# Performance work log

Hardware: AMD Instinct MI355X
Metric: run time of the kernel (lower is better)

The kernel has to match this reference:

```python
import jax, jax.numpy as jnp
import numpy as np

B, F, D, H = 2048, 32, 64, 64

def setup_inputs() -> dict:
    key = jax.random.key(0)
    k1, k2, k3 = jax.random.split(key, 3)
    x = jax.random.normal(k1, (B, F, D), dtype=jnp.float32)
    W1 = jax.random.normal(k2, (D, H), dtype=jnp.float32) * 0.01
    b1 = jnp.zeros((H,), dtype=jnp.float32)
    Ws = jax.random.normal(k3, (H, 1), dtype=jnp.float32) * 0.01
    bs = jnp.zeros((1,), dtype=jnp.float32)
    return {"x": x, "W1": W1, "b1": b1, "Ws": Ws, "bs": bs}

def reference(x, W1, b1, Ws, bs):
    # pairwise field interactions: cross[b, p, d] = x[b, i_p, d] * x[b, j_p, d]
    f = x.shape[1]
    ii, jj = np.triu_indices(f, k=1)  # P = f*(f-1)/2 pairs
    cross = x[:, ii, :] * x[:, jj, :]            # [B, P, D]
    # small MLP (DNN with one hidden layer, relu, dropout disabled in eval)
    h = jax.nn.relu(jnp.einsum('bpd,dh->bph', cross, W1) + b1)  # [B, P, H]
    # attention score per pair, softmax over pairs
    scores = (jnp.einsum('bph,ho->bpo', h, Ws) + bs).squeeze(-1)  # [B, P]
    attn = jax.nn.softmax(scores, axis=-1)                        # [B, P]
    pool = jnp.sum(cross * attn[:, :, None], axis=1)              # [B, D]
    afm = jnp.sum(pool, axis=1, keepdims=True)                    # [B, 1]
    return afm
```

## Files before the change

### kernel.cpp

```cpp
#include <hip/hip_runtime.h>


#define F 32
#define D 64
#define H 64
#define P 496
#define NT 4
#define MT 32
#define RB 72

typedef __attribute__((ext_vector_type(8))) _Float16 f16x8;
typedef __attribute__((ext_vector_type(2))) _Float16 f16x2;
typedef __attribute__((ext_vector_type(4))) float f32x4;

__global__ __launch_bounds__(256, 4) void afm_kernel(
    const float* __restrict__ x, const float* __restrict__ W1,
    const float* __restrict__ b1, const float* __restrict__ Ws,
    const float* __restrict__ bs, float* __restrict__ out)
{
    __shared__ _Float16 xs[F * RB];
    __shared__ int   pairtab[512];
    __shared__ float scores[512];
    __shared__ float svals[512];
    __shared__ float redmax[4], rednum[4], redden[4];

    const int tid  = threadIdx.x;
    const int b    = blockIdx.x;
    const int lane = tid & 63;
    const int wid  = tid >> 6;
    const int l15  = lane & 15;
    const int quad = lane >> 4;

    const float4* xb4 = (const float4*)(x + (size_t)b * (F * D));
    for (int v = tid; v < (F * D) / 4; v += 256) {
        float4 w = xb4[v];
        int row = v >> 4, col = (v & 15) * 4;
        f16x2 lo = { (_Float16)w.x, (_Float16)w.y };
        f16x2 hi = { (_Float16)w.z, (_Float16)w.w };
        *(f16x2*)&xs[row * RB + col]     = lo;
        *(f16x2*)&xs[row * RB + col + 2] = hi;
    }
    for (int p = tid; p < 512; p += 256) {
        int i, j;
        if (p < P) {
            i = (int)((63.0f - __builtin_sqrtf((float)(3969 - 8 * p))) * 0.5f);
            if (i * (63 - i) / 2 > p) --i;
            if ((i + 1) * (62 - i) / 2 <= p) ++i;
            j = i + 1 + (p - i * (63 - i) / 2);
        } else { i = 0; j = 0; }
        pairtab[p] = (i * RB * 2) << 16 | (j * RB * 2);
    }
    const float bsv = bs[0];

    f16x8 wfrag[NT][2];
    #pragma unroll
    for (int nt = 0; nt < NT; ++nt)
        #pragma unroll
        for (int ks = 0; ks < 2; ++ks)
            #pragma unroll
            for (int j8 = 0; j8 < 8; ++j8) {
                int k = quad * 8 + j8 + ks * 32;
                wfrag[nt][ks][j8] = (_Float16)W1[k * H + nt * 16 + l15];
            }
    const _Float16 onev = (l15 == 0) ? (_Float16)1.0f : (_Float16)0.0f;
    const f16x8 onesf = {onev, onev, onev, onev, onev, onev, onev, onev};

    float breg[16], wreg[16];
    #pragma unroll
    for (int nt = 0; nt < NT; ++nt)
        #pragma unroll
        for (int reg = 0; reg < 4; ++reg) {
            int n = nt * 16 + quad * 4 + reg;
            breg[nt * 4 + reg] = b1[n];
            wreg[nt * 4 + reg] = Ws[n];
        }
    __syncthreads();

    const char* xsb = (const char*)xs;
    const int qb = quad << 4;

    for (int t = wid; t < MT; t += 4) {
        const int p0 = t * 16;
        const int pk = pairtab[p0 + l15];
        const int io = ((unsigned)pk) >> 16;
        const int jo = pk & 0xFFFF;

        f16x8 xi0 = *(const f16x8*)(xsb + io + qb);
        f16x8 xj0 = *(const f16x8*)(xsb + jo + qb);
        f16x8 xi1 = *(const f16x8*)(xsb + io + 64 + qb);
        f16x8 xj1 = *(const f16x8*)(xsb + jo + 64 + qb);

        f16x8 A0 = xi0 * xj0;
        f16x8 A1 = xi1 * xj1;

        f32x4 acc[NT];
        #pragma unroll
        for (int nt = 0; nt < NT; ++nt) { f32x4 z = {0.f,0.f,0.f,0.f}; acc[nt] = z; }
        f32x4 accs = {0.f, 0.f, 0.f, 0.f};

        #pragma unroll
        for (int nt = 0; nt < NT; ++nt)
            acc[nt] = __builtin_amdgcn_mfma_f32_16x16x32_f16(wfrag[nt][0], A0, acc[nt], 0, 0, 0);
        accs = __builtin_amdgcn_mfma_f32_16x16x32_f16(onesf, A0, accs, 0, 0, 0);
        #pragma unroll
        for (int nt = 0; nt < NT; ++nt)
            acc[nt] = __builtin_amdgcn_mfma_f32_16x16x32_f16(wfrag[nt][1], A1, acc[nt], 0, 0, 0);
        accs = __builtin_amdgcn_mfma_f32_16x16x32_f16(onesf, A1, accs, 0, 0, 0);

        float s = 0.f;
        #pragma unroll
        for (int nt = 0; nt < NT; ++nt)
            #pragma unroll
            for (int reg = 0; reg < 4; ++reg) {
                float v = acc[nt][reg] + breg[nt * 4 + reg];
                v = v > 0.f ? v : 0.f;
                s = fmaf(v, wreg[nt * 4 + reg], s);
            }
        s += __shfl_xor(s, 16, 64);
        s += __shfl_xor(s, 32, 64);
        if (quad == 0) {
            scores[p0 + l15] = s + bsv;
            svals[p0 + l15]  = accs[0];
        }
    }
    __syncthreads();

    float m = -1e30f;
    for (int p = tid; p < P; p += 256) m = fmaxf(m, scores[p]);
    #pragma unroll
    for (int off = 32; off >= 1; off >>= 1) m = fmaxf(m, __shfl_xor(m, off, 64));
    if (lane == 0) redmax[wid] = m;
    __syncthreads();
    m = fmaxf(fmaxf(redmax[0], redmax[1]), fmaxf(redmax[2], redmax[3]));

    float num = 0.f, den = 0.f;
    for (int p = tid; p < P; p += 256) {
        float e = __expf(scores[p] - m);
        num += e * svals[p];
        den += e;
    }
    #pragma unroll
    for (int off = 32; off >= 1; off >>= 1) {
        num += __shfl_xor(num, off, 64);
        den += __shfl_xor(den, off, 64);
    }
    if (lane == 0) { rednum[wid] = num; redden[wid] = den; }
    __syncthreads();
    if (tid == 0) {
        float nn = rednum[0] + rednum[1] + rednum[2] + rednum[3];
        float dd = redden[0] + redden[1] + redden[2] + redden[3];
        out[b] = nn / dd;
    }
}

extern "C" void kernel_launch(void* const* d_in, const int* in_sizes, int n_in,
                              void* d_out, int out_size, void* d_ws, size_t ws_size,
                              hipStream_t stream) {
    const float* x  = (const float*)d_in[0];
    const float* W1 = (const float*)d_in[1];
    const float* b1 = (const float*)d_in[2];
    const float* Ws = (const float*)d_in[3];
    const float* bs = (const float*)d_in[4];
    float* out = (float*)d_out;
    const int B = in_sizes[0] / (F * D);
    afm_kernel<<<B, 256, 0, stream>>>(x, W1, b1, Ws, bs, out);
}
```

Baseline: 83.91 us.

## Restructure pair loop over row-i tiles and drop max-subtracted softmax

Replaces the shared-memory staging of x and the pair table with direct global loads into registers. Each wave iterates over row i and builds 16-column j tiles of products, masking out pairs with j <= i. The separate max pass of the softmax is removed, so exp is applied to raw scores and num/den are accumulated in registers without score buffers or most barriers. This cuts LDS traffic and synchronisation but computes some masked pairs that are thrown away, and drops overflow protection in the exponent, relying on scores staying small.

```diff
diff --git a/kernel.cpp b/kernel.cpp
--- a/kernel.cpp
+++ b/kernel.cpp
@@ -4,25 +4,16 @@
 #define F 32
 #define D 64
 #define H 64
-#define P 496
-#define NT 4
-#define MT 32
-#define RB 72
 
 typedef __attribute__((ext_vector_type(8))) _Float16 f16x8;
-typedef __attribute__((ext_vector_type(2))) _Float16 f16x2;
 typedef __attribute__((ext_vector_type(4))) float f32x4;
 
-__global__ __launch_bounds__(256, 4) void afm_kernel(
+__global__ __launch_bounds__(256, 3) void afm_kernel(
     const float* __restrict__ x, const float* __restrict__ W1,
     const float* __restrict__ b1, const float* __restrict__ Ws,
     const float* __restrict__ bs, float* __restrict__ out)
 {
-    __shared__ _Float16 xs[F * RB];
-    __shared__ int   pairtab[512];
-    __shared__ float scores[512];
-    __shared__ float svals[512];
-    __shared__ float redmax[4], rednum[4], redden[4];
+    __shared__ float rednum[4], redden[4];
 
     const int tid  = threadIdx.x;
     const int b    = blockIdx.x;
@@ -31,116 +22,104 @@
     const int l15  = lane & 15;
     const int quad = lane >> 4;
 
-    const float4* xb4 = (const float4*)(x + (size_t)b * (F * D));
-    for (int v = tid; v < (F * D) / 4; v += 256) {
-        float4 w = xb4[v];
-        int row = v >> 4, col = (v & 15) * 4;
-        f16x2 lo = { (_Float16)w.x, (_Float16)w.y };
-        f16x2 hi = { (_Float16)w.z, (_Float16)w.w };
-        *(f16x2*)&xs[row * RB + col]     = lo;
-        *(f16x2*)&xs[row * RB + col + 2] = hi;
-    }
-    for (int p = tid; p < 512; p += 256) {
-        int i, j;
-        if (p < P) {
-            i = (int)((63.0f - __builtin_sqrtf((float)(3969 - 8 * p))) * 0.5f);
-            if (i * (63 - i) / 2 > p) --i;
-            if ((i + 1) * (62 - i) / 2 <= p) ++i;
-            j = i + 1 + (p - i * (63 - i) / 2);
-        } else { i = 0; j = 0; }
-        pairtab[p] = (i * RB * 2) << 16 | (j * RB * 2);
-    }
-    const float bsv = bs[0];
-
-    f16x8 wfrag[NT][2];
+    f16x8 wfrag[4][2];
     #pragma unroll
-    for (int nt = 0; nt < NT; ++nt)
+    for (int nt = 0; nt < 4; ++nt)
         #pragma unroll
         for (int ks = 0; ks < 2; ++ks)
             #pragma unroll
-            for (int j8 = 0; j8 < 8; ++j8) {
-                int k = quad * 8 + j8 + ks * 32;
-                wfrag[nt][ks][j8] = (_Float16)W1[k * H + nt * 16 + l15];
-            }
+            for (int j8 = 0; j8 < 8; ++j8)
+                wfrag[nt][ks][j8] =
+                    (_Float16)W1[(quad * 8 + j8 + 32 * ks) * H + nt * 16 + l15];
+
     const _Float16 onev = (l15 == 0) ? (_Float16)1.0f : (_Float16)0.0f;
     const f16x8 onesf = {onev, onev, onev, onev, onev, onev, onev, onev};
 
     float breg[16], wreg[16];
     #pragma unroll
-    for (int nt = 0; nt < NT; ++nt)
+    for (int nt = 0; nt < 4; ++nt)
         #pragma unroll
         for (int reg = 0; reg < 4; ++reg) {
             int n = nt * 16 + quad * 4 + reg;
             breg[nt * 4 + reg] = b1[n];
             wreg[nt * 4 + reg] = Ws[n];
         }
-    __syncthreads();
+    const float bsv = bs[0];
 
-    const char* xsb = (const char*)xs;
-    const int qb = quad << 4;
+    const float* xb = x + (size_t)b * (F * D);
+    f16x8 xjf[2][2];
+    #pragma unroll
+    for (int J = 0; J < 2; ++J)
+        #pragma unroll
+        for (int ks = 0; ks < 2; ++ks) {
+            const float* src = xb + (J * 16 + l15) * D + quad * 8 + 32 * ks;
+            float4 a = *(const float4*)src;
+            float4 c = *(const float4*)(src + 4);
+            f16x8 v;
+            v[0] = (_Float16)a.x; v[1] = (_Float16)a.y;
+            v[2] = (_Float16)a.z; v[3] = (_Float16)a.w;
+            v[4] = (_Float16)c.x; v[5] = (_Float16)c.y;
+            v[6] = (_Float16)c.z; v[7] = (_Float16)c.w;
+            xjf[J][ks] = v;
+        }
 
-    for (int t = wid; t < MT; t += 4) {
-        const int p0 = t * 16;
-        const int pk = pairtab[p0 + l15];
-        const int io = ((unsigned)pk) >> 16;
-        const int jo = pk & 0xFFFF;
+    float num = 0.f, den = 0.f;
 
-        f16x8 xi0 = *(const f16x8*)(xsb + io + qb);
-        f16x8 xj0 = *(const f16x8*)(xsb + jo + qb);
-        f16x8 xi1 = *(const f16x8*)(xsb + io + 64 + qb);
-        f16x8 xj1 = *(const f16x8*)(xsb + jo + 64 + qb);
+    for (int ii = 0; ii < 8; ++ii) {
+        const int i = wid + 4 * ii;
 
-        f16x8 A0 = xi0 * xj0;
-        f16x8 A1 = xi1 * xj1;
+        f16x8 xi16[2];
+        #pragma unroll
+        for (int ks = 0; ks < 2; ++ks) {
+            const float* src = xb + i * D + quad * 8 + 32 * ks;
+            float4 a = *(const float4*)src;
+            float4 c = *(const float4*)(src + 4);
+            f16x8 v;
+            v[0] = (_Float16)a.x; v[1] = (_Float16)a.y;
+            v[2] = (_Float16)a.z; v[3] = (_Float16)a.w;
+            v[4] = (_Float16)c.x; v[5] = (_Float16)c.y;
+            v[6] = (_Float16)c.z; v[7] = (_Float16)c.w;
+            xi16[ks] = v;
+        }
 
-        f32x4 acc[NT];
-        #pragma unroll
-        for (int nt = 0; nt < NT; ++nt) { f32x4 z = {0.f,0.f,0.f,0.f}; acc[nt] = z; }
-        f32x4 accs = {0.f, 0.f, 0.f, 0.f};
+        for (int Jp = (i < 16) ? 0 : 1; Jp < 2; ++Jp) {
+            f32x4 acc[4];
+            #pragma unroll
+            for (int nt = 0; nt < 4; ++nt) { f32x4 z = {0.f,0.f,0.f,0.f}; acc[nt] = z; }
+            f32x4 accs = {0.f, 0.f, 0.f, 0.f};
 
-        #pragma unroll
-        for (int nt = 0; nt < NT; ++nt)
-            acc[nt] = __builtin_amdgcn_mfma_f32_16x16x32_f16(wfrag[nt][0], A0, acc[nt], 0, 0, 0);
-        accs = __builtin_amdgcn_mfma_f32_16x16x32_f16(onesf, A0, accs, 0, 0, 0);
-        #pragma unroll
-        for (int nt = 0; nt < NT; ++nt)
-            acc[nt] = __builtin_amdgcn_mfma_f32_16x16x32_f16(wfrag[nt][1], A1, acc[nt], 0, 0, 0);
-        accs = __builtin_amdgcn_mfma_f32_16x16x32_f16(onesf, A1, accs, 0, 0, 0);
+            #pragma unroll
+            for (int ks = 0; ks < 2; ++ks) {
+                f16x8 B = xjf[Jp][ks] * xi16[ks];
+                #pragma unroll
+                for (int nt = 0; nt < 4; ++nt)
+                    acc[nt] = __builtin_amdgcn_mfma_f32_16x16x32_f16(
+                                  wfrag[nt][ks], B, acc[nt], 0, 0, 0);
+                accs = __builtin_amdgcn_mfma_f32_16x16x32_f16(onesf, B, accs, 0, 0, 0);
+            }
 
-        float s = 0.f;
-        #pragma unroll
-        for (int nt = 0; nt < NT; ++nt)
+            float s = 0.f;
             #pragma unroll
-            for (int reg = 0; reg < 4; ++reg) {
-                float v = acc[nt][reg] + breg[nt * 4 + reg];
-                v = v > 0.f ? v : 0.f;
-                s = fmaf(v, wreg[nt * 4 + reg], s);
-            }
-        s += __shfl_xor(s, 16, 64);
-        s += __shfl_xor(s, 32, 64);
-        if (quad == 0) {
-            scores[p0 + l15] = s + bsv;
-            svals[p0 + l15]  = accs[0];
+            for (int nt = 0; nt < 4; ++nt)
+                #pragma unroll
+                for (int reg = 0; reg < 4; ++reg) {
+                    float v = acc[nt][reg] + breg[nt * 4 + reg];
+                    v = v > 0.f ? v : 0.f;
+                    s = fmaf(v, wreg[nt * 4 + reg], s);
+                }
+            s += __shfl_xor(s, 16, 64);
+            s += __shfl_xor(s, 32, 64);
+
+            float e = __expf(s + bsv);
+            const int j = Jp * 16 + l15;
+            e = (quad == 0 && j > i) ? e : 0.f;
+            num = fmaf(e, accs[0], num);
+            den += e;
         }
     }
-    __syncthreads();
 
-    float m = -1e30f;
-    for (int p = tid; p < P; p += 256) m = fmaxf(m, scores[p]);
     #pragma unroll
-    for (int off = 32; off >= 1; off >>= 1) m = fmaxf(m, __shfl_xor(m, off, 64));
-    if (lane == 0) redmax[wid] = m;
-    __syncthreads();
-    m = fmaxf(fmaxf(redmax[0], redmax[1]), fmaxf(redmax[2], redmax[3]));
-
-    float num = 0.f, den = 0.f;
-    for (int p = tid; p < P; p += 256) {
-        float e = __expf(scores[p] - m);
-        num += e * svals[p];
-        den += e;
-    }
-    #pragma unroll
-    for (int off = 32; off >= 1; off >>= 1) {
+    for (int off = 8; off >= 1; off >>= 1) {
         num += __shfl_xor(num, off, 64);
         den += __shfl_xor(den, off, 64);
     }
```

Measured after the change: 95.05 us. +13.3%, slower.

## Fuse softmax into MFMA loop, stage W1 fragments via LDS, pack bias math

Applied to the files above, without the earlier changes.

Drops the max-subtraction pass and the scores/svals shared arrays. Exp and the numerator/denominator sums are now accumulated directly inside the pair loop, which removes two block barriers and the extra LDS passes. W1 is loaded once with coalesced float4 reads into a fragment-ordered LDS buffer instead of strided scalar global loads per lane. The bias, relu and score step uses packed float2 math. Skipping max subtraction risks overflow in exp if scores grow large; with the small weights in the test inputs the scores stay near zero.

```diff
diff --git a/kernel.cpp b/kernel.cpp
--- a/kernel.cpp
+++ b/kernel.cpp
@@ -5,13 +5,13 @@
 #define D 64
 #define H 64
 #define P 496
-#define NT 4
 #define MT 32
 #define RB 72
 
 typedef __attribute__((ext_vector_type(8))) _Float16 f16x8;
 typedef __attribute__((ext_vector_type(2))) _Float16 f16x2;
 typedef __attribute__((ext_vector_type(4))) float f32x4;
+typedef __attribute__((ext_vector_type(2))) float f32x2;
 
 __global__ __launch_bounds__(256, 4) void afm_kernel(
     const float* __restrict__ x, const float* __restrict__ W1,
@@ -19,10 +19,10 @@
     const float* __restrict__ bs, float* __restrict__ out)
 {
     __shared__ _Float16 xs[F * RB];
-    __shared__ int   pairtab[512];
-    __shared__ float scores[512];
-    __shared__ float svals[512];
-    __shared__ float redmax[4], rednum[4], redden[4];
+    __shared__ _Float16 w1f[4096];
+    __shared__ float2 bw[H];
+    __shared__ int pairtab[512];
+    __shared__ float rednum[4], redden[4];
 
     const int tid  = threadIdx.x;
     const int b    = blockIdx.x;
@@ -40,6 +40,22 @@
         *(f16x2*)&xs[row * RB + col]     = lo;
         *(f16x2*)&xs[row * RB + col + 2] = hi;
     }
+    const float4* w14 = (const float4*)W1;
+    #pragma unroll
+    for (int s = 0; s < 4; ++s) {
+        int v = tid + s * 256;
+        float4 w = w14[v];
+        int k  = v >> 4;
+        int ks = k >> 5, kq = (k >> 3) & 3, j8 = k & 7;
+        int n0 = (v & 15) * 4;
+        float e4[4] = { w.x, w.y, w.z, w.w };
+        #pragma unroll
+        for (int c = 0; c < 4; ++c) {
+            int n = n0 + c, nt = n >> 4, l = n & 15;
+            w1f[(((ks * 4 + nt) * 16 + l) * 4 + kq) * 8 + j8] = (_Float16)e4[c];
+        }
+    }
+    if (tid < H) bw[tid] = make_float2(b1[tid], Ws[tid]);
     for (int p = tid; p < 512; p += 256) {
         int i, j;
         if (p < P) {
@@ -51,33 +67,31 @@
         pairtab[p] = (i * RB * 2) << 16 | (j * RB * 2);
     }
     const float bsv = bs[0];
+    __syncthreads();
 
-    f16x8 wfrag[NT][2];
+    f16x8 wfrag[4][2];
     #pragma unroll
-    for (int nt = 0; nt < NT; ++nt)
+    for (int nt = 0; nt < 4; ++nt)
         #pragma unroll
         for (int ks = 0; ks < 2; ++ks)
-            #pragma unroll
-            for (int j8 = 0; j8 < 8; ++j8) {
-                int k = quad * 8 + j8 + ks * 32;
-                wfrag[nt][ks][j8] = (_Float16)W1[k * H + nt * 16 + l15];
-            }
+            wfrag[nt][ks] = *(const f16x8*)&w1f[(((ks * 4 + nt) * 16 + l15) * 4 + quad) * 8];
+
     const _Float16 onev = (l15 == 0) ? (_Float16)1.0f : (_Float16)0.0f;
     const f16x8 onesf = {onev, onev, onev, onev, onev, onev, onev, onev};
 
-    float breg[16], wreg[16];
+    f32x2 b2[8], w2[8];
     #pragma unroll
-    for (int nt = 0; nt < NT; ++nt)
-        #pragma unroll
-        for (int reg = 0; reg < 4; ++reg) {
-            int n = nt * 16 + quad * 4 + reg;
-            breg[nt * 4 + reg] = b1[n];
-            wreg[nt * 4 + reg] = Ws[n];
-        }
-    __syncthreads();
+    for (int nt = 0; nt < 4; ++nt) {
+        const float2* src = &bw[nt * 16 + quad * 4];
+        float2 q0 = src[0], q1 = src[1], q2 = src[2], q3 = src[3];
+        b2[nt*2+0] = (f32x2){q0.x, q1.x}; w2[nt*2+0] = (f32x2){q0.y, q1.y};
+        b2[nt*2+1] = (f32x2){q2.x, q3.x}; w2[nt*2+1] = (f32x2){q2.y, q3.y};
+    }
 
     const char* xsb = (const char*)xs;
     const int qb = quad << 4;
+    float num = 0.f, den = 0.f;
+    const f32x2 z2 = {0.f, 0.f};
 
     for (int t = wid; t < MT; t += 4) {
         const int p0 = t * 16;
@@ -93,54 +107,43 @@
         f16x8 A0 = xi0 * xj0;
         f16x8 A1 = xi1 * xj1;
 
-        f32x4 acc[NT];
+        f32x4 acc[4];
         #pragma unroll
-        for (int nt = 0; nt < NT; ++nt) { f32x4 z = {0.f,0.f,0.f,0.f}; acc[nt] = z; }
+        for (int nt = 0; nt < 4; ++nt) { f32x4 z = {0.f,0.f,0.f,0.f}; acc[nt] = z; }
         f32x4 accs = {0.f, 0.f, 0.f, 0.f};
 
         #pragma unroll
-        for (int nt = 0; nt < NT; ++nt)
+        for (int nt = 0; nt < 4; ++nt)
             acc[nt] = __builtin_amdgcn_mfma_f32_16x16x32_f16(wfrag[nt][0], A0, acc[nt], 0, 0, 0);
         accs = __builtin_amdgcn_mfma_f32_16x16x32_f16(onesf, A0, accs, 0, 0, 0);
         #pragma unroll
-        for (int nt = 0; nt < NT; ++nt)
+        for (int nt = 0; nt < 4; ++nt)
             acc[nt] = __builtin_amdgcn_mfma_f32_16x16x32_f16(wfrag[nt][1], A1, acc[nt], 0, 0, 0);
         accs = __builtin_amdgcn_mfma_f32_16x16x32_f16(onesf, A1, accs, 0, 0, 0);
 
-        float s = 0.f;
+        f32x2 s2 = {0.f, 0.f};
         #pragma unroll
-        for (int nt = 0; nt < NT; ++nt)
-            #pragma unroll
-            for (int reg = 0; reg < 4; ++reg) {
-                float v = acc[nt][reg] + breg[nt * 4 + reg];
-                v = v > 0.f ? v : 0.f;
-                s = fmaf(v, wreg[nt * 4 + reg], s);
-            }
+        for (int nt = 0; nt < 4; ++nt) {
+            f32x2 lo = {acc[nt][0], acc[nt][1]};
+            f32x2 hi = {acc[nt][2], acc[nt][3]};
+            lo += b2[nt*2+0]; hi += b2[nt*2+1];
+            lo = __builtin_elementwise_max(lo, z2);
+            hi = __builtin_elementwise_max(hi, z2);
+            s2 = lo * w2[nt*2+0] + s2;
+            s2 = hi * w2[nt*2+1] + s2;
+        }
+        float s = s2.x + s2.y;
         s += __shfl_xor(s, 16, 64);
         s += __shfl_xor(s, 32, 64);
-        if (quad == 0) {
-            scores[p0 + l15] = s + bsv;
-            svals[p0 + l15]  = accs[0];
-        }
-    }
-    __syncthreads();
 
-    float m = -1e30f;
-    for (int p = tid; p < P; p += 256) m = fmaxf(m, scores[p]);
-    #pragma unroll
-    for (int off = 32; off >= 1; off >>= 1) m = fmaxf(m, __shfl_xor(m, off, 64));
-    if (lane == 0) redmax[wid] = m;
-    __syncthreads();
-    m = fmaxf(fmaxf(redmax[0], redmax[1]), fmaxf(redmax[2], redmax[3]));
-
-    float num = 0.f, den = 0.f;
-    for (int p = tid; p < P; p += 256) {
-        float e = __expf(scores[p] - m);
-        num += e * svals[p];
+        float e = __expf(s + bsv);
+        e = (quad == 0 && p0 + l15 < P) ? e : 0.f;
+        num = fmaf(e, accs[0], num);
         den += e;
     }
+
     #pragma unroll
-    for (int off = 32; off >= 1; off >>= 1) {
+    for (int off = 8; off >= 1; off >>= 1) {
         num += __shfl_xor(num, off, 64);
         den += __shfl_xor(den, off, 64);
     }
```

Result: slower. 86.77 us (+3.4%).
